# Performance work log

Measured on AMD Instinct MI355X. Metric: run time of the kernel, lower is better.

Reference implementation:

```python
import jax, jax.numpy as jnp
import numpy as np

PI = jnp.pi

def phasor_encode(x):
    # map phase in [-1,1] to unit complex phasor exp(i*pi*x)
    return jnp.exp(jnp.complex64(1j) * PI * x.astype(jnp.float32))

def phasor_act(z):
    # angle of complex activation, normalized back to [-1,1]
    return jnp.angle(z) / PI

def multi_dense(x, w, b):
    # PhasorMultiDense: x [b,t,d], w [h,d,D], b [h,D] (complex bias, ones init)
    xz = phasor_encode(x)                                      # [b,t,d] complex64
    wz = w.astype(jnp.complex64)
    bz = b.astype(jnp.complex64)
    yz = jnp.einsum('btd,hdD->bhtD', xz, wz) + bz[None, :, None, :]
    return phasor_act(yz)                                      # [b,h,t,D] real

def attend(q, k, v):
    # VSA phasor attention: similarity = Re(qz . conj(kz)) / d, softmax, complex bundle of v phasors
    d = q.shape[-1]
    qz = phasor_encode(q)
    kz = phasor_encode(k)
    scores = jnp.real(jnp.einsum('bhtd,bhTd->bhtT', qz, jnp.conj(kz))) / d
    probs = jax.nn.softmax(scores, axis=-1)
    vz = phasor_encode(v)
    out = jnp.einsum('bhtT,bhTd->bhtd', probs.astype(jnp.complex64), vz)
    return phasor_act(out)                                     # [b,h,t,D]

def setup_inputs() -> dict:
    key = jax.random.key(0)
    ks = jax.random.split(key, 8)
    B, Tq, Tkv, D, H = 2, 1024, 1024, 512, 8
    sw = 1.0 / np.sqrt(D)       # VarianceScaling(1.0) fan_in
    swo = 1.0 / np.sqrt(H * D)
    return {
        'query': jax.random.uniform(ks[0], (B, Tq, D), jnp.float32, -1.0, 1.0),
        'keyvalue': jax.random.uniform(ks[1], (B, Tkv, D), jnp.float32, -1.0, 1.0),
        'wq': jax.random.normal(ks[2], (H, D, D), jnp.float32) * sw,
        'bq': jnp.ones((H, D), jnp.float32),
        'wk': jax.random.normal(ks[3], (H, D, D), jnp.float32) * sw,
        'bk': jnp.ones((H, D), jnp.float32),
        'wv': jax.random.normal(ks[4], (H, D, D), jnp.float32) * sw,
        'bv': jnp.ones((H, D), jnp.float32),
        'wo': jax.random.normal(ks[5], (H * D, D), jnp.float32) * swo,
        'bo': jnp.ones((D,), jnp.float32),
    }

def reference(query, keyvalue, wq, bq, wk, bk, wv, bv, wo, bo):
    q = multi_dense(query, wq, bq)        # [b,h,t,D]
    k = multi_dense(keyvalue, wk, bk)
    v = multi_dense(keyvalue, wv, bv)
    r = attend(q, k, v)                   # [b,h,t,D]
    b_, h_, t_, d_ = r.shape
    r_flat = jnp.transpose(r, (0, 2, 1, 3)).reshape(b_, t_, h_ * d_)  # b t (h d)
    # final PhasorDense
    xz = phasor_encode(r_flat)
    z = jnp.einsum('btd,dD->btD', xz, wo.astype(jnp.complex64)) + bo.astype(jnp.complex64)
    return phasor_act(z)                  # [b, t_q, output_channels]
```

## Files before the change

### kernel.cpp

```cpp
#include <hip/hip_runtime.h>
#include <math.h>


#define PI_F 3.14159274101257324f

typedef __attribute__((ext_vector_type(8))) _Float16 half8;
typedef __attribute__((ext_vector_type(4))) _Float16 half4;
typedef __attribute__((ext_vector_type(2))) _Float16 half2v;
typedef __attribute__((ext_vector_type(16))) float f32x16;
typedef unsigned int u32;

#define MFMA32(a, b, c) __builtin_amdgcn_mfma_f32_32x32x16_f16((a), (b), (c), 0, 0, 0)
#define ROWOF(r, ln) (((r) & 3) + 8 * ((r) >> 2) + 4 * ((ln) >> 5))

__device__ __forceinline__ void gll16(const void* g, void* l) {
    __builtin_amdgcn_global_load_lds(
        (const __attribute__((address_space(1))) u32*)g,
        (__attribute__((address_space(3))) u32*)l, 16, 0, 0);
}

#define MKSRC(U, NT, gh, gl, stride, sp, dp, dbase)                         \
    _Pragma("unroll") for (int u_ = 0; u_ < (U); ++u_) {                    \
        const int idx_ = u_ * (NT) + tid;                                   \
        const int row_ = idx_ >> 3, ss_ = idx_ & 7;                         \
        const int sl_ = ss_ ^ (row_ & 7);                                   \
        sp[u_] = ((sl_ < 4) ? (gh) : (gl)) + (size_t)row_ * (stride)        \
                 + (sl_ & 3) * 8;                                           \
        dp[u_] = (dbase) + idx_ * 16;                                       \
    }
#define STAGE(U, sp, dp, bufoff, kk)                                        \
    _Pragma("unroll") for (int u_ = 0; u_ < (U); ++u_)                      \
        gll16(sp[u_] + (kk), lds + (bufoff) + dp[u_]);

__device__ __forceinline__ half8 fragP(const char* ldsp, int row, int oct, int hilo) {
    const int sl = (oct + hilo * 4) ^ (row & 7);
    return *(const half8*)(ldsp + row * 128 + (sl << 4));
}

__device__ __forceinline__ void split2(float x, _Float16& h, _Float16& l) {
    _Float16 hh = (_Float16)x;
    h = hh;
    l = (_Float16)((x - (float)hh) * 4096.0f);
}

__device__ __forceinline__ int xcdswz(int bid, int nwg) {
    const int cpx = nwg >> 3;
    return (bid & 7) * cpx + (bid >> 3);
}

__global__ __launch_bounds__(256) void encode_phasor(
    const float* __restrict__ x,
    _Float16* __restrict__ ch, _Float16* __restrict__ cl,
    _Float16* __restrict__ sh, _Float16* __restrict__ sl)
{
    const int idx = blockIdx.x * 256 + threadIdx.x;
    float4 v = ((const float4*)x)[idx];
    float cc[4], ss[4];
    sincosf(PI_F * v.x, &ss[0], &cc[0]);
    sincosf(PI_F * v.y, &ss[1], &cc[1]);
    sincosf(PI_F * v.z, &ss[2], &cc[2]);
    sincosf(PI_F * v.w, &ss[3], &cc[3]);
    half4 chv, clv, shv, slv;
#pragma unroll
    for (int q = 0; q < 4; ++q) {
        _Float16 a, b;
        split2(cc[q], a, b); chv[q] = a; clv[q] = b;
        split2(ss[q], a, b); shv[q] = a; slv[q] = b;
    }
    ((half4*)ch)[idx] = chv;
    ((half4*)cl)[idx] = clv;
    ((half4*)sh)[idx] = shv;
    ((half4*)sl)[idx] = slv;
}

__global__ __launch_bounds__(256) void tsplit64(
    const float* __restrict__ w, _Float16* __restrict__ th, _Float16* __restrict__ tl,
    int K, int N)
{
    const int kt = blockIdx.x, ntile = blockIdx.y, h = blockIdx.z;
    const int k0 = kt * 64, n0 = ntile * 64;
    __shared__ float T[64][65];
    const int tid = threadIdx.x;
    const float* wb = w + (size_t)h * K * N;
    {
        const int r = tid >> 4, c4 = (tid & 15) * 4;
#pragma unroll
        for (int rr = 0; rr < 64; rr += 16) {
            float4 v = *(const float4*)&wb[(size_t)(k0 + rr + r) * N + n0 + c4];
            T[rr + r][c4 + 0] = v.x; T[rr + r][c4 + 1] = v.y;
            T[rr + r][c4 + 2] = v.z; T[rr + r][c4 + 3] = v.w;
        }
    }
    __syncthreads();
    {
        const int n = tid >> 2, kq = (tid & 3) * 16;
        half8 hv[2], lv[2];
#pragma unroll
        for (int q = 0; q < 16; ++q) {
            float f = T[kq + q][n];
            _Float16 hh, ll; split2(f, hh, ll);
            hv[q >> 3][q & 7] = hh; lv[q >> 3][q & 7] = ll;
        }
        _Float16* oh = th + ((size_t)h * N + n0 + n) * K + k0 + kq;
        _Float16* ol = tl + ((size_t)h * N + n0 + n) * K + k0 + kq;
        *(half8*)oh = hv[0]; *(half8*)(oh + 8) = hv[1];
        *(half8*)ol = lv[0]; *(half8*)(ol + 8) = lv[1];
    }
}

__global__ __launch_bounds__(256, 2) void proj_qk(
    const _Float16* __restrict__ qch, const _Float16* __restrict__ qcl,
    const _Float16* __restrict__ qsh, const _Float16* __restrict__ qsl,
    const _Float16* __restrict__ kch, const _Float16* __restrict__ kcl,
    const _Float16* __restrict__ ksh, const _Float16* __restrict__ ksl,
    const _Float16* __restrict__ wqh, const _Float16* __restrict__ wql,
    const _Float16* __restrict__ wkh, const _Float16* __restrict__ wkl,
    const float* __restrict__ bq, const float* __restrict__ bk,
    _Float16* __restrict__ qzh, _Float16* __restrict__ qzl,
    _Float16* __restrict__ kzh, _Float16* __restrict__ kzl,
    int h0, int hcnt)
{
    const int inp = blockIdx.z;
    const _Float16* xch = inp ? kch : qch;
    const _Float16* xcl = inp ? kcl : qcl;
    const _Float16* xsh = inp ? ksh : qsh;
    const _Float16* xsl = inp ? ksl : qsl;
    const _Float16* wth = inp ? wkh : wqh;
    const _Float16* wtl = inp ? wkl : wql;
    const float* bias = inp ? bk : bq;
    _Float16* ozh = inp ? kzh : qzh;
    _Float16* ozl = inp ? kzl : qzl;

    const int m0 = blockIdx.x * 64;
    const int hc = blockIdx.y >> 2;
    const int n0 = (blockIdx.y & 3) * 128;
    __shared__ char lds[65536];
    const int tid = threadIdx.x, wv = tid >> 6, ln = tid & 63;
    const int wr = wv >> 1, wc = wv & 1, lm32 = ln & 31, lh = ln >> 5;

    const _Float16* sp_xc[2]; int dp_xc[2];
    const _Float16* sp_xs[2]; int dp_xs[2];
    const _Float16* sp_w[4];  int dp_w[4];
    MKSRC(2, 256, xch + (size_t)m0 * 512, xcl + (size_t)m0 * 512, 512, sp_xc, dp_xc, 0);
    MKSRC(2, 256, xsh + (size_t)m0 * 512, xsl + (size_t)m0 * 512, 512, sp_xs, dp_xs, 8192);
    const _Float16* wbh = wth + ((size_t)hc * 512 + n0) * 512;
    const _Float16* wbl = wtl + ((size_t)hc * 512 + n0) * 512;
    MKSRC(4, 256, wbh, wbl, 512, sp_w, dp_w, 16384);

    f32x16 ach[2] = {}, acl[2] = {}, ash[2] = {}, asl[2] = {};

    STAGE(2, sp_xc, dp_xc, 0, 0);
    STAGE(2, sp_xs, dp_xs, 0, 0);
    STAGE(4, sp_w,  dp_w,  0, 0);
    int off = 0;
    for (int s = 0; s < 16; ++s) {
        __syncthreads();
        const int nxt = off ^ 32768;
        if (s + 1 < 16) {
            const int kk = (s + 1) * 32;
            STAGE(2, sp_xc, dp_xc, nxt, kk);
            STAGE(2, sp_xs, dp_xs, nxt, kk);
            STAGE(4, sp_w,  dp_w,  nxt, kk);
        }
        const char* Xc = lds + off;
        const char* Xs = lds + off + 8192;
        const char* W  = lds + off + 16384;
        __builtin_amdgcn_s_setprio(1);
#pragma unroll
        for (int kw = 0; kw < 2; ++kw) {
            const int oct = kw * 2 + lh;
            half8 wh0 = fragP(W, wc * 64 + lm32, oct, 0);
            half8 wh1 = fragP(W, wc * 64 + 32 + lm32, oct, 0);
            half8 wl0 = fragP(W, wc * 64 + lm32, oct, 1);
            half8 wl1 = fragP(W, wc * 64 + 32 + lm32, oct, 1);
            half8 c1 = fragP(Xc, wr * 32 + lm32, oct, 0);
            half8 c2 = fragP(Xc, wr * 32 + lm32, oct, 1);
            half8 s1 = fragP(Xs, wr * 32 + lm32, oct, 0);
            half8 s2 = fragP(Xs, wr * 32 + lm32, oct, 1);
            ach[0] = MFMA32(c1, wh0, ach[0]);
            acl[0] = MFMA32(c1, wl0, acl[0]);
            acl[0] = MFMA32(c2, wh0, acl[0]);
            ash[0] = MFMA32(s1, wh0, ash[0]);
            asl[0] = MFMA32(s1, wl0, asl[0]);
            asl[0] = MFMA32(s2, wh0, asl[0]);
            ach[1] = MFMA32(c1, wh1, ach[1]);
            acl[1] = MFMA32(c1, wl1, acl[1]);
            acl[1] = MFMA32(c2, wh1, acl[1]);
            ash[1] = MFMA32(s1, wh1, ash[1]);
            asl[1] = MFMA32(s1, wl1, asl[1]);
            asl[1] = MFMA32(s2, wh1, asl[1]);
        }
        __builtin_amdgcn_s_setprio(0);
        off = nxt;
    }

    const float LS = 1.0f / 4096.0f;
    const int b = m0 >> 10, tbase = m0 & 1023;
    const size_t zz = (size_t)(b * hcnt + hc);
#pragma unroll
    for (int j = 0; j < 2; ++j) {
        const int nloc = wc * 64 + j * 32 + lm32;
        const float bval = bias[(size_t)(h0 + hc) * 512 + n0 + nloc];
#pragma unroll
        for (int r = 0; r < 16; ++r) {
            const int mloc = wr * 32 + ROWOF(r, ln);
            float yc = ach[j][r] + acl[j][r] * LS + bval;
            float ys = ash[j][r] + asl[j][r] * LS;
            float inv = 1.0f / sqrtf(fmaxf(yc * yc + ys * ys, 1e-36f));
            float c = yc * inv, sn = ys * inv;
            _Float16 chh, chl, shh, shl;
            split2(c, chh, chl); split2(sn, shh, shl);
            const size_t offo = (zz * 1024 + tbase + mloc) * 1024 + 2 * (n0 + nloc);
            half2v hv, lv;
            hv[0] = chh; hv[1] = shh; lv[0] = chl; lv[1] = shl;
            *(half2v*)(ozh + offo) = hv;
            *(half2v*)(ozl + offo) = lv;
        }
    }
}

__global__ __launch_bounds__(256, 2) void proj_v(
    const _Float16* __restrict__ xch, const _Float16* __restrict__ xcl,
    const _Float16* __restrict__ xsh, const _Float16* __restrict__ xsl,
    const _Float16* __restrict__ wth, const _Float16* __restrict__ wtl,
    const float* __restrict__ bias,
    _Float16* __restrict__ vch, _Float16* __restrict__ vcl,
    _Float16* __restrict__ vsh, _Float16* __restrict__ vsl,
    int h0, int hcnt)
{
    const int m0 = blockIdx.x * 64;
    const int hc = blockIdx.y >> 2;
    const int n0 = (blockIdx.y & 3) * 128;
    __shared__ char lds[65536];
    const int tid = threadIdx.x, wv = tid >> 6, ln = tid & 63;
    const int wr = wv >> 1, wc = wv & 1, lm32 = ln & 31, lh = ln >> 5;

    const _Float16* sp_xc[2]; int dp_xc[2];
    const _Float16* sp_xs[2]; int dp_xs[2];
    const _Float16* sp_w[4];  int dp_w[4];
    MKSRC(2, 256, xch + (size_t)m0 * 512, xcl + (size_t)m0 * 512, 512, sp_xc, dp_xc, 0);
    MKSRC(2, 256, xsh + (size_t)m0 * 512, xsl + (size_t)m0 * 512, 512, sp_xs, dp_xs, 8192);
    const _Float16* wbh = wth + ((size_t)hc * 512 + n0) * 512;
    const _Float16* wbl = wtl + ((size_t)hc * 512 + n0) * 512;
    MKSRC(4, 256, wbh, wbl, 512, sp_w, dp_w, 16384);

    f32x16 ach[2] = {}, acl[2] = {}, ash[2] = {}, asl[2] = {};

    STAGE(2, sp_xc, dp_xc, 0, 0);
    STAGE(2, sp_xs, dp_xs, 0, 0);
    STAGE(4, sp_w,  dp_w,  0, 0);
    int off = 0;
    for (int s = 0; s < 16; ++s) {
        __syncthreads();
        const int nxt = off ^ 32768;
        if (s + 1 < 16) {
            const int kk = (s + 1) * 32;
            STAGE(2, sp_xc, dp_xc, nxt, kk);
            STAGE(2, sp_xs, dp_xs, nxt, kk);
            STAGE(4, sp_w,  dp_w,  nxt, kk);
        }
        const char* Xc = lds + off;
        const char* Xs = lds + off + 8192;
        const char* W  = lds + off + 16384;
        __builtin_amdgcn_s_setprio(1);
#pragma unroll
        for (int kw = 0; kw < 2; ++kw) {
            const int oct = kw * 2 + lh;
            half8 wh0 = fragP(W, wc * 64 + lm32, oct, 0);
            half8 wh1 = fragP(W, wc * 64 + 32 + lm32, oct, 0);
            half8 wl0 = fragP(W, wc * 64 + lm32, oct, 1);
            half8 wl1 = fragP(W, wc * 64 + 32 + lm32, oct, 1);
            half8 c1 = fragP(Xc, wr * 32 + lm32, oct, 0);
            half8 c2 = fragP(Xc, wr * 32 + lm32, oct, 1);
            half8 s1 = fragP(Xs, wr * 32 + lm32, oct, 0);
            half8 s2 = fragP(Xs, wr * 32 + lm32, oct, 1);
            ach[0] = MFMA32(c1, wh0, ach[0]);
            acl[0] = MFMA32(c1, wl0, acl[0]);
            acl[0] = MFMA32(c2, wh0, acl[0]);
            ash[0] = MFMA32(s1, wh0, ash[0]);
            asl[0] = MFMA32(s1, wl0, asl[0]);
            asl[0] = MFMA32(s2, wh0, asl[0]);
            ach[1] = MFMA32(c1, wh1, ach[1]);
            acl[1] = MFMA32(c1, wl1, acl[1]);
            acl[1] = MFMA32(c2, wh1, acl[1]);
            ash[1] = MFMA32(s1, wh1, ash[1]);
            asl[1] = MFMA32(s1, wl1, asl[1]);
            asl[1] = MFMA32(s2, wh1, asl[1]);
        }
        __builtin_amdgcn_s_setprio(0);
        off = nxt;
    }

    const float LS = 1.0f / 4096.0f;
    const int b = m0 >> 10, tbase = m0 & 1023;
    const size_t zz = (size_t)(b * hcnt + hc);
    _Float16* T = (_Float16*)lds;
#pragma unroll
    for (int round = 0; round < 2; ++round) {
        __syncthreads();
#pragma unroll
        for (int j = 0; j < 2; ++j) {
            const int dloc = wc * 64 + j * 32 + lm32;
            const float bval = bias[(size_t)(h0 + hc) * 512 + n0 + dloc];
#pragma unroll
            for (int r = 0; r < 16; ++r) {
                const int tloc = wr * 32 + ROWOF(r, ln);
                float yc = ach[j][r] + acl[j][r] * LS + bval;
                float ys = ash[j][r] + asl[j][r] * LS;
                float inv = 1.0f / sqrtf(fmaxf(yc * yc + ys * ys, 1e-36f));
                float val = (round ? ys : yc) * inv;
                _Float16 hh, ll;
                split2(val, hh, ll);
                T[dloc * 72 + tloc] = hh;
                T[9216 + dloc * 72 + tloc] = ll;
            }
        }
        __syncthreads();
        {
            const int p2 = tid >> 7, d = tid & 127;
            const _Float16* src = T + p2 * 9216 + d * 72;
            _Float16* plane = (round == 0) ? (p2 ? vcl : vch) : (p2 ? vsl : vsh);
            _Float16* dst = plane + (zz * 512 + n0 + d) * 1024 + tbase;
#pragma unroll
            for (int q = 0; q < 8; ++q)
                *(half8*)(dst + q * 8) = *(const half8*)(src + q * 8);
        }
    }
}

__global__ __launch_bounds__(256, 2) void scores_mfma(
    const _Float16* __restrict__ qzh, const _Float16* __restrict__ qzl,
    const _Float16* __restrict__ kzh, const _Float16* __restrict__ kzl,
    float* __restrict__ S, int Z)
{
    const int wg = xcdswz(blockIdx.x, Z * 64);
    const int z = wg >> 6;
    const int rem = wg & 63;
    const int m0 = (rem & 7) << 7, n0 = (rem >> 3) << 7;
    __shared__ char lds[65536];
    const size_t zb = (size_t)z << 20;
    const int tid = threadIdx.x, wv = tid >> 6, ln = tid & 63;
    const int wr = wv >> 1, wc = wv & 1, lm32 = ln & 31, lh = ln >> 5;

    const _Float16* sp_a[4]; int dp_a[4];
    const _Float16* sp_b[4]; int dp_b[4];
    MKSRC(4, 256, qzh + zb + (size_t)m0 * 1024, qzl + zb + (size_t)m0 * 1024, 1024, sp_a, dp_a, 0);
    MKSRC(4, 256, kzh + zb + (size_t)n0 * 1024, kzl + zb + (size_t)n0 * 1024, 1024, sp_b, dp_b, 16384);

    f32x16 acch[2][2] = {}, accl[2][2] = {};

    STAGE(4, sp_a, dp_a, 0, 0);
    STAGE(4, sp_b, dp_b, 0, 0);
    int off = 0;
    for (int s = 0; s < 32; ++s) {
        __syncthreads();
        const int nxt = off ^ 32768;
        if (s + 1 < 32) {
            const int kk = (s + 1) * 32;
            STAGE(4, sp_a, dp_a, nxt, kk);
            STAGE(4, sp_b, dp_b, nxt, kk);
        }
        const char* A  = lds + off;
        const char* Bb = lds + off + 16384;
        __builtin_amdgcn_s_setprio(1);
#pragma unroll
        for (int kw = 0; kw < 2; ++kw) {
            const int oct = kw * 2 + lh;
            half8 bh0 = fragP(Bb, wc * 64 + lm32, oct, 0);
            half8 bh1 = fragP(Bb, wc * 64 + 32 + lm32, oct, 0);
            half8 bl0 = fragP(Bb, wc * 64 + lm32, oct, 1);
            half8 bl1 = fragP(Bb, wc * 64 + 32 + lm32, oct, 1);
#pragma unroll
            for (int i = 0; i < 2; ++i) {
                half8 qh = fragP(A, wr * 64 + i * 32 + lm32, oct, 0);
                half8 ql = fragP(A, wr * 64 + i * 32 + lm32, oct, 1);
                acch[i][0] = MFMA32(qh, bh0, acch[i][0]);
                accl[i][0] = MFMA32(qh, bl0, accl[i][0]);
                accl[i][0] = MFMA32(ql, bh0, accl[i][0]);
                acch[i][1] = MFMA32(qh, bh1, acch[i][1]);
                accl[i][1] = MFMA32(qh, bl1, accl[i][1]);
                accl[i][1] = MFMA32(ql, bh1, accl[i][1]);
            }
        }
        __builtin_amdgcn_s_setprio(0);
        off = nxt;
    }
    const float LS = 1.0f / 4096.0f, SC = 1.0f / 512.0f;
#pragma unroll
    for (int i = 0; i < 2; ++i)
#pragma unroll
        for (int j = 0; j < 2; ++j)
#pragma unroll
            for (int r = 0; r < 16; ++r) {
                const int row = m0 + wr * 64 + i * 32 + ROWOF(r, ln);
                const int col = n0 + wc * 64 + j * 32 + lm32;
                S[zb + (size_t)row * 1024 + col] =
                    (acch[i][j][r] + accl[i][j][r] * LS) * SC;
            }
}

__global__ __launch_bounds__(256) void softmax_split(float* __restrict__ S)
{
    const size_t row = blockIdx.x;
    float* p = S + row * 1024;
    const int tid = threadIdx.x;
    float4 v = ((const float4*)p)[tid];
    float m = fmaxf(fmaxf(v.x, v.y), fmaxf(v.z, v.w));
#pragma unroll
    for (int off = 32; off >= 1; off >>= 1)
        m = fmaxf(m, __shfl_xor(m, off));
    __shared__ float redm[4], reds[4];
    const int wid = tid >> 6, lane = tid & 63;
    if (lane == 0) redm[wid] = m;
    __syncthreads();
    m = fmaxf(fmaxf(redm[0], redm[1]), fmaxf(redm[2], redm[3]));
    float4 e;
    e.x = expf(v.x - m); e.y = expf(v.y - m);
    e.z = expf(v.z - m); e.w = expf(v.w - m);
    float s = (e.x + e.y) + (e.z + e.w);
#pragma unroll
    for (int off = 32; off >= 1; off >>= 1)
        s += __shfl_xor(s, off);
    if (lane == 0) reds[wid] = s;
    __syncthreads();
    s = (reds[0] + reds[1]) + (reds[2] + reds[3]);
    e.x /= s; e.y /= s; e.z /= s; e.w /= s;
    __syncthreads();
    _Float16* ph = (_Float16*)p;
    half4 hv, lv;
    _Float16 a, b;
    split2(e.x, a, b); hv[0] = a; lv[0] = b;
    split2(e.y, a, b); hv[1] = a; lv[1] = b;
    split2(e.z, a, b); hv[2] = a; lv[2] = b;
    split2(e.w, a, b); hv[3] = a; lv[3] = b;
    *(half4*)(ph + tid * 4) = hv;
    *(half4*)(ph + 1024 + tid * 4) = lv;
}

__global__ __launch_bounds__(256, 2) void pv_mfma(
    const _Float16* __restrict__ P,
    const _Float16* __restrict__ vch, const _Float16* __restrict__ vcl,
    const _Float16* __restrict__ vsh, const _Float16* __restrict__ vsl,
    _Float16* __restrict__ rch, _Float16* __restrict__ rcl,
    _Float16* __restrict__ rsh, _Float16* __restrict__ rsl,
    int h0, int hcnt, int Z)
{
    const int wg = xcdswz(blockIdx.x, Z * 64);
    const int z = wg >> 6;
    const int rem = wg & 63;
    const int m0 = (rem & 7) << 7, n0 = (rem >> 3) << 6;
    __shared__ char lds[65536];
    const int tid = threadIdx.x, wv = tid >> 6, ln = tid & 63;
    const int wr = wv >> 1, wc = wv & 1, lm32 = ln & 31, lh = ln >> 5;

    const _Float16* Pb = P + (size_t)z * 1024 * 2048 + (size_t)m0 * 2048;
    const size_t vb = (size_t)z * 512 * 1024 + (size_t)n0 * 1024;
    const _Float16* sp_p[4];  int dp_p[4];
    const _Float16* sp_vc[2]; int dp_vc[2];
    const _Float16* sp_vs[2]; int dp_vs[2];
    MKSRC(4, 256, Pb, Pb + 1024, 2048, sp_p, dp_p, 0);
    MKSRC(2, 256, vch + vb, vcl + vb, 1024, sp_vc, dp_vc, 16384);
    MKSRC(2, 256, vsh + vb, vsl + vb, 1024, sp_vs, dp_vs, 24576);

    f32x16 ac_h[2] = {}, ac_l[2] = {}, as_h[2] = {}, as_l[2] = {};

    STAGE(4, sp_p,  dp_p,  0, 0);
    STAGE(2, sp_vc, dp_vc, 0, 0);
    STAGE(2, sp_vs, dp_vs, 0, 0);
    int off = 0;
    for (int s = 0; s < 32; ++s) {
        __syncthreads();
        const int nxt = off ^ 32768;
        if (s + 1 < 32) {
            const int kk = (s + 1) * 32;
            STAGE(4, sp_p,  dp_p,  nxt, kk);
            STAGE(2, sp_vc, dp_vc, nxt, kk);
            STAGE(2, sp_vs, dp_vs, nxt, kk);
        }
        const char* A  = lds + off;
        const char* Vc = lds + off + 16384;
        const char* Vs = lds + off + 24576;
        __builtin_amdgcn_s_setprio(1);
#pragma unroll
        for (int kw = 0; kw < 2; ++kw) {
            const int oct = kw * 2 + lh;
            half8 vc1 = fragP(Vc, wc * 32 + lm32, oct, 0);
            half8 vc2 = fragP(Vc, wc * 32 + lm32, oct, 1);
            half8 vs1 = fragP(Vs, wc * 32 + lm32, oct, 0);
            half8 vs2 = fragP(Vs, wc * 32 + lm32, oct, 1);
#pragma unroll
            for (int i = 0; i < 2; ++i) {
                half8 ph = fragP(A, wr * 64 + i * 32 + lm32, oct, 0);
                half8 pl = fragP(A, wr * 64 + i * 32 + lm32, oct, 1);
                ac_h[i] = MFMA32(ph, vc1, ac_h[i]);
                ac_l[i] = MFMA32(ph, vc2, ac_l[i]);
                ac_l[i] = MFMA32(pl, vc1, ac_l[i]);
                as_h[i] = MFMA32(ph, vs1, as_h[i]);
                as_l[i] = MFMA32(ph, vs2, as_l[i]);
                as_l[i] = MFMA32(pl, vs1, as_l[i]);
            }
        }
        __builtin_amdgcn_s_setprio(0);
        off = nxt;
    }
    const float LS = 1.0f / 4096.0f;
    const int b = z / hcnt, hg = h0 + z % hcnt;
#pragma unroll
    for (int i = 0; i < 2; ++i)
#pragma unroll
        for (int r = 0; r < 16; ++r) {
            const int t = m0 + wr * 64 + i * 32 + ROWOF(r, ln);
            const int d = n0 + wc * 32 + lm32;
            float zc = ac_h[i][r] + ac_l[i][r] * LS;
            float zs = as_h[i][r] + as_l[i][r] * LS;
            float inv = 1.0f / sqrtf(fmaxf(zc * zc + zs * zs, 1e-36f));
            float c = zc * inv, sn = zs * inv;
            _Float16 chh, chl, shh, shl;
            split2(c, chh, chl); split2(sn, shh, shl);
            const size_t offo = ((size_t)(b * 1024 + t)) * 4096 + (size_t)hg * 512 + d;
            rch[offo] = chh; rcl[offo] = chl; rsh[offo] = shh; rsl[offo] = shl;
        }
}

__global__ __launch_bounds__(256, 2) void final_mfma(
    const _Float16* __restrict__ rch, const _Float16* __restrict__ rcl,
    const _Float16* __restrict__ rsh, const _Float16* __restrict__ rsl,
    const _Float16* __restrict__ woh, const _Float16* __restrict__ wol,
    float* __restrict__ pbuf)
{
    const int m0 = blockIdx.x * 64, n0 = blockIdx.y * 128;
    const int ks = blockIdx.z;
    const size_t kbase = (size_t)ks * 1024;
    __shared__ char lds[65536];
    const int tid = threadIdx.x, wv = tid >> 6, ln = tid & 63;
    const int wr = wv >> 1, wc = wv & 1, lm32 = ln & 31, lh = ln >> 5;

    const _Float16* sp_rc[2]; int dp_rc[2];
    const _Float16* sp_rs[2]; int dp_rs[2];
    const _Float16* sp_w[4];  int dp_w[4];
    MKSRC(2, 256, rch + (size_t)m0 * 4096 + kbase, rcl + (size_t)m0 * 4096 + kbase, 4096, sp_rc, dp_rc, 0);
    MKSRC(2, 256, rsh + (size_t)m0 * 4096 + kbase, rsl + (size_t)m0 * 4096 + kbase, 4096, sp_rs, dp_rs, 8192);
    MKSRC(4, 256, woh + (size_t)n0 * 4096 + kbase, wol + (size_t)n0 * 4096 + kbase, 4096, sp_w, dp_w, 16384);

    f32x16 rr_h[2] = {}, rr_l[2] = {}, ri_h[2] = {}, ri_l[2] = {};

    STAGE(2, sp_rc, dp_rc, 0, 0);
    STAGE(2, sp_rs, dp_rs, 0, 0);
    STAGE(4, sp_w,  dp_w,  0, 0);
    int off = 0;
    for (int s = 0; s < 32; ++s) {
        __syncthreads();
        const int nxt = off ^ 32768;
        if (s + 1 < 32) {
            const int kk = (s + 1) * 32;
            STAGE(2, sp_rc, dp_rc, nxt, kk);
            STAGE(2, sp_rs, dp_rs, nxt, kk);
            STAGE(4, sp_w,  dp_w,  nxt, kk);
        }
        const char* Rc = lds + off;
        const char* Rs = lds + off + 8192;
        const char* W  = lds + off + 16384;
        __builtin_amdgcn_s_setprio(1);
#pragma unroll
        for (int kw = 0; kw < 2; ++kw) {
            const int oct = kw * 2 + lh;
            half8 wh0 = fragP(W, wc * 64 + lm32, oct, 0);
            half8 wh1 = fragP(W, wc * 64 + 32 + lm32, oct, 0);
            half8 wl0 = fragP(W, wc * 64 + lm32, oct, 1);
            half8 wl1 = fragP(W, wc * 64 + 32 + lm32, oct, 1);
            half8 c1 = fragP(Rc, wr * 32 + lm32, oct, 0);
            half8 c2 = fragP(Rc, wr * 32 + lm32, oct, 1);
            half8 s1 = fragP(Rs, wr * 32 + lm32, oct, 0);
            half8 s2 = fragP(Rs, wr * 32 + lm32, oct, 1);
            rr_h[0] = MFMA32(c1, wh0, rr_h[0]);
            rr_l[0] = MFMA32(c1, wl0, rr_l[0]);
            rr_l[0] = MFMA32(c2, wh0, rr_l[0]);
            ri_h[0] = MFMA32(s1, wh0, ri_h[0]);
            ri_l[0] = MFMA32(s1, wl0, ri_l[0]);
            ri_l[0] = MFMA32(s2, wh0, ri_l[0]);
            rr_h[1] = MFMA32(c1, wh1, rr_h[1]);
            rr_l[1] = MFMA32(c1, wl1, rr_l[1]);
            rr_l[1] = MFMA32(c2, wh1, rr_l[1]);
            ri_h[1] = MFMA32(s1, wh1, ri_h[1]);
            ri_l[1] = MFMA32(s1, wl1, ri_l[1]);
            ri_l[1] = MFMA32(s2, wh1, ri_l[1]);
        }
        __builtin_amdgcn_s_setprio(0);
        off = nxt;
    }
    const float LS = 1.0f / 4096.0f;
#pragma unroll
    for (int j = 0; j < 2; ++j) {
        const int ng = n0 + wc * 64 + j * 32 + lm32;
#pragma unroll
        for (int r = 0; r < 16; ++r) {
            const int mg = m0 + wr * 32 + ROWOF(r, ln);
            float zr = rr_h[j][r] + rr_l[j][r] * LS;
            float zi = ri_h[j][r] + ri_l[j][r] * LS;
            float2 v; v.x = zr; v.y = zi;
            *(float2*)&pbuf[((size_t)(ks * 2048 + mg) * 512 + ng) * 2] = v;
        }
    }
}

__global__ __launch_bounds__(256) void final_combine(
    const float* __restrict__ pbuf, const float* __restrict__ bo,
    float* __restrict__ out, int KS)
{
    const int m = blockIdx.x, t = threadIdx.x;
    float4 acc = {0.f, 0.f, 0.f, 0.f};
    for (int s = 0; s < KS; ++s) {
        float4 v = *(const float4*)&pbuf[(size_t)(s * 2048 + m) * 1024 + t * 4];
        acc.x += v.x; acc.y += v.y; acc.z += v.z; acc.w += v.w;
    }
    const int n0 = t * 2;
    out[(size_t)m * 512 + n0]     = atan2f(acc.y, acc.x + bo[n0]) / PI_F;
    out[(size_t)m * 512 + n0 + 1] = atan2f(acc.w, acc.z + bo[n0 + 1]) / PI_F;
}

extern "C" void kernel_launch(void* const* d_in, const int* in_sizes, int n_in,
                              void* d_out, int out_size, void* d_ws, size_t ws_size,
                              hipStream_t stream)
{
    (void)in_sizes; (void)n_in; (void)out_size;
    const float* query    = (const float*)d_in[0];
    const float* keyvalue = (const float*)d_in[1];
    const float* wq = (const float*)d_in[2];
    const float* bq = (const float*)d_in[3];
    const float* wk = (const float*)d_in[4];
    const float* bk = (const float*)d_in[5];
    const float* wv = (const float*)d_in[6];
    const float* bv = (const float*)d_in[7];
    const float* wo = (const float*)d_in[8];
    const float* bo = (const float*)d_in[9];
    float* out = (float*)d_out;

    int hcnt;
    if (ws_size >= (size_t)320 * 1024 * 1024) hcnt = 8;
    else if (ws_size >= (size_t)240 * 1024 * 1024) hcnt = 4;
    else hcnt = 2;
    const int Z = 2 * hcnt;
    const int KS = (hcnt == 2) ? 2 : 4;

    char* p = (char*)d_ws;
    auto alloc = [&](size_t bytes) {
        char* r = p;
        p += (bytes + 255) & ~(size_t)255;
        return r;
    };
    const size_t PLX = (size_t)2048 * 512;
    _Float16* xq[4]; for (int i = 0; i < 4; ++i) xq[i] = (_Float16*)alloc(PLX * 2);
    _Float16* xk[4]; for (int i = 0; i < 4; ++i) xk[i] = (_Float16*)alloc(PLX * 2);
    _Float16* woT[2]; for (int i = 0; i < 2; ++i) woT[i] = (_Float16*)alloc((size_t)512 * 4096 * 2);
    const size_t WTE = (size_t)hcnt * 512 * 512;
    _Float16* wqT[2]; for (int i = 0; i < 2; ++i) wqT[i] = (_Float16*)alloc(WTE * 2);
    _Float16* wkT[2]; for (int i = 0; i < 2; ++i) wkT[i] = (_Float16*)alloc(WTE * 2);
    _Float16* wvT[2]; for (int i = 0; i < 2; ++i) wvT[i] = (_Float16*)alloc(WTE * 2);
    const size_t QZE = (size_t)Z * 1024 * 1024;
    _Float16* qz[2]; for (int i = 0; i < 2; ++i) qz[i] = (_Float16*)alloc(QZE * 2);
    _Float16* kz[2]; for (int i = 0; i < 2; ++i) kz[i] = (_Float16*)alloc(QZE * 2);
    float* S = (float*)alloc(QZE * 4);
    const size_t VTE = (size_t)Z * 512 * 1024;
    _Float16* vT[4]; for (int i = 0; i < 4; ++i) vT[i] = (_Float16*)alloc(VTE * 2);
    const size_t RCE = (size_t)2048 * 4096;
    _Float16* rcs[4];
    if (hcnt == 8) {
        for (int i = 0; i < 4; ++i) rcs[i] = (_Float16*)((char*)qz[0] + (size_t)i * RCE * 2);
    } else {
        for (int i = 0; i < 4; ++i) rcs[i] = (_Float16*)alloc(RCE * 2);
    }
    float* pbuf = (float*)kz[0];

    dim3 blk(256);

    encode_phasor<<<1024, blk, 0, stream>>>(query, xq[0], xq[1], xq[2], xq[3]);
    encode_phasor<<<1024, blk, 0, stream>>>(keyvalue, xk[0], xk[1], xk[2], xk[3]);
    tsplit64<<<dim3(64, 8, 1), blk, 0, stream>>>(wo, woT[0], woT[1], 4096, 512);

    for (int c = 0; c < 8 / hcnt; ++c) {
        const int h0 = c * hcnt;
        const float* wqc = wq + (size_t)h0 * 512 * 512;
        const float* wkc = wk + (size_t)h0 * 512 * 512;
        const float* wvc = wv + (size_t)h0 * 512 * 512;
        tsplit64<<<dim3(8, 8, hcnt), blk, 0, stream>>>(wqc, wqT[0], wqT[1], 512, 512);
        tsplit64<<<dim3(8, 8, hcnt), blk, 0, stream>>>(wkc, wkT[0], wkT[1], 512, 512);
        tsplit64<<<dim3(8, 8, hcnt), blk, 0, stream>>>(wvc, wvT[0], wvT[1], 512, 512);

        proj_qk<<<dim3(32, 4 * hcnt, 2), blk, 0, stream>>>(
            xq[0], xq[1], xq[2], xq[3], xk[0], xk[1], xk[2], xk[3],
            wqT[0], wqT[1], wkT[0], wkT[1], bq, bk,
            qz[0], qz[1], kz[0], kz[1], h0, hcnt);
        proj_v<<<dim3(32, 4 * hcnt), blk, 0, stream>>>(
            xk[0], xk[1], xk[2], xk[3], wvT[0], wvT[1], bv,
            vT[0], vT[1], vT[2], vT[3], h0, hcnt);

        scores_mfma<<<dim3(Z * 64), blk, 0, stream>>>(qz[0], qz[1], kz[0], kz[1], S, Z);
        softmax_split<<<dim3(Z * 1024), blk, 0, stream>>>(S);
        pv_mfma<<<dim3(Z * 64), blk, 0, stream>>>(
            (const _Float16*)S, vT[0], vT[1], vT[2], vT[3],
            rcs[0], rcs[1], rcs[2], rcs[3], h0, hcnt, Z);
    }

    final_mfma<<<dim3(32, 4, KS), blk, 0, stream>>>(
        rcs[0], rcs[1], rcs[2], rcs[3], woT[0], woT[1], pbuf);
    final_combine<<<dim3(2048), blk, 0, stream>>>(pbuf, bo, out, KS);
}
```

Measured before the change: 579.9 us.

## Use 512-thread blocks with triple-buffered LDS pipeline in all MFMA GEMM kernels

All the MFMA GEMM kernels (projections, scores, PV, final) now use 512-thread blocks with wider N tiles. Staging moves from a double-buffered swizzled layout to a three-slot ring of pre-fragmented LDS tiles, prefetched three k-steps ahead with explicit vmcnt waits and split barriers. Each k-step's fragments go into registers before the next prefetch is issued. This aims to hide global-load latency and halve redundant reloads of the X tiles, at the cost of 144KB of LDS per block, which likely caps occupancy at one block per CU despite the launch bound of 2. It also raises register pressure.

```diff
diff --git a/kernel.cpp b/kernel.cpp
--- a/kernel.cpp
+++ b/kernel.cpp
@@ -19,24 +19,6 @@
         (__attribute__((address_space(3))) u32*)l, 16, 0, 0);
 }
 
-#define MKSRC(U, NT, gh, gl, stride, sp, dp, dbase)                         \
-    _Pragma("unroll") for (int u_ = 0; u_ < (U); ++u_) {                    \
-        const int idx_ = u_ * (NT) + tid;                                   \
-        const int row_ = idx_ >> 3, ss_ = idx_ & 7;                         \
-        const int sl_ = ss_ ^ (row_ & 7);                                   \
-        sp[u_] = ((sl_ < 4) ? (gh) : (gl)) + (size_t)row_ * (stride)        \
-                 + (sl_ & 3) * 8;                                           \
-        dp[u_] = (dbase) + idx_ * 16;                                       \
-    }
-#define STAGE(U, sp, dp, bufoff, kk)                                        \
-    _Pragma("unroll") for (int u_ = 0; u_ < (U); ++u_)                      \
-        gll16(sp[u_] + (kk), lds + (bufoff) + dp[u_]);
-
-__device__ __forceinline__ half8 fragP(const char* ldsp, int row, int oct, int hilo) {
-    const int sl = (oct + hilo * 4) ^ (row & 7);
-    return *(const half8*)(ldsp + row * 128 + (sl << 4));
-}
-
 __device__ __forceinline__ void split2(float x, _Float16& h, _Float16& l) {
     _Float16 hh = (_Float16)x;
     h = hh;
@@ -47,6 +29,26 @@
     const int cpx = nwg >> 3;
     return (bid & 7) * cpx + (bid >> 3);
 }
+
+#define SLOT 49152
+
+#define ISSUE6(slotoff, kk)                                                  \
+    _Pragma("unroll") for (int u_ = 0; u_ < 6; ++u_)                         \
+        gll16(sp[u_] + (kk), lds + (slotoff) + dp[u_]);
+
+#define PIPE_WAIT(s, NS)                                                     \
+    if ((s) + 3 <= (NS))      asm volatile("s_waitcnt vmcnt(12)" ::: "memory"); \
+    else if ((s) + 2 == (NS)) asm volatile("s_waitcnt vmcnt(6)" ::: "memory");  \
+    else                      asm volatile("s_waitcnt vmcnt(0)" ::: "memory");  \
+    __builtin_amdgcn_s_barrier();                                            \
+    __builtin_amdgcn_sched_barrier(0);
+
+#define PIPE_MID(s, NS)                                                      \
+    asm volatile("s_waitcnt lgkmcnt(0)" ::: "memory");                       \
+    __builtin_amdgcn_sched_barrier(0);                                       \
+    __builtin_amdgcn_s_barrier();                                            \
+    __builtin_amdgcn_sched_barrier(0);                                       \
+    if ((s) + 3 < (NS)) { ISSUE6(off, ((s) + 3) * 64); }
 
 __global__ __launch_bounds__(256) void encode_phasor(
     const float* __restrict__ x,
@@ -108,7 +110,7 @@
     }
 }
 
-__global__ __launch_bounds__(256, 2) void proj_qk(
+__global__ __launch_bounds__(512, 2) void proj_qk(
     const _Float16* __restrict__ qch, const _Float16* __restrict__ qcl,
     const _Float16* __restrict__ qsh, const _Float16* __restrict__ qsl,
     const _Float16* __restrict__ kch, const _Float16* __restrict__ kcl,
@@ -132,66 +134,64 @@
     _Float16* ozl = inp ? kzl : qzl;
 
     const int m0 = blockIdx.x * 64;
-    const int hc = blockIdx.y >> 2;
-    const int n0 = (blockIdx.y & 3) * 128;
-    __shared__ char lds[65536];
+    const int hc = blockIdx.y >> 1;
+    const int n0h = (blockIdx.y & 1) * 256;
+    __shared__ char lds[147456];
     const int tid = threadIdx.x, wv = tid >> 6, ln = tid & 63;
-    const int wr = wv >> 1, wc = wv & 1, lm32 = ln & 31, lh = ln >> 5;
-
-    const _Float16* sp_xc[2]; int dp_xc[2];
-    const _Float16* sp_xs[2]; int dp_xs[2];
-    const _Float16* sp_w[4];  int dp_w[4];
-    MKSRC(2, 256, xch + (size_t)m0 * 512, xcl + (size_t)m0 * 512, 512, sp_xc, dp_xc, 0);
-    MKSRC(2, 256, xsh + (size_t)m0 * 512, xsl + (size_t)m0 * 512, 512, sp_xs, dp_xs, 8192);
-    const _Float16* wbh = wth + ((size_t)hc * 512 + n0) * 512;
-    const _Float16* wbl = wtl + ((size_t)hc * 512 + n0) * 512;
-    MKSRC(4, 256, wbh, wbl, 512, sp_w, dp_w, 16384);
+    const int wr = wv >> 2, wc = wv & 3, lm32 = ln & 31;
+
+    const char* sp[6]; int dp[6];
+#pragma unroll
+    for (int u = 0; u < 6; ++u) {
+        const int g = u * 8 + wv;
+        const _Float16 *ph, *pl; int row0, stride; int f;
+        if (g < 8)       { f = g;      ph = xch; pl = xcl; row0 = m0; stride = 512; }
+        else if (g < 16) { f = g - 8;  ph = xsh; pl = xsl; row0 = m0; stride = 512; }
+        else             { f = g - 16;
+                           ph = wth + (size_t)hc * 262144;
+                           pl = wtl + (size_t)hc * 262144;
+                           row0 = n0h; stride = 512; }
+        const int R = f >> 2, ks = (f >> 1) & 1, hl = f & 1;
+        sp[u] = (const char*)((hl ? pl : ph)
+                + (size_t)(row0 + R * 32 + (ln & 31)) * stride
+                + ks * 16 + (ln >> 5) * 8);
+        dp[u] = u * 8192 + tid * 16;
+    }
 
     f32x16 ach[2] = {}, acl[2] = {}, ash[2] = {}, asl[2] = {};
 
-    STAGE(2, sp_xc, dp_xc, 0, 0);
-    STAGE(2, sp_xs, dp_xs, 0, 0);
-    STAGE(4, sp_w,  dp_w,  0, 0);
+    ISSUE6(0, 0); ISSUE6(SLOT, 64); ISSUE6(2 * SLOT, 128);
     int off = 0;
-    for (int s = 0; s < 16; ++s) {
-        __syncthreads();
-        const int nxt = off ^ 32768;
-        if (s + 1 < 16) {
-            const int kk = (s + 1) * 32;
-            STAGE(2, sp_xc, dp_xc, nxt, kk);
-            STAGE(2, sp_xs, dp_xs, nxt, kk);
-            STAGE(4, sp_w,  dp_w,  nxt, kk);
-        }
-        const char* Xc = lds + off;
-        const char* Xs = lds + off + 8192;
-        const char* W  = lds + off + 16384;
+    const int NS = 16;
+    for (int s = 0; s < NS; ++s) {
+        PIPE_WAIT(s, NS);
+        half8 xc[2][2], xs[2][2], w[2][2][2];
+#pragma unroll
+        for (int ks = 0; ks < 2; ++ks)
+#pragma unroll
+            for (int hl = 0; hl < 2; ++hl) {
+                xc[ks][hl] = *(const half8*)(lds + off + (wr * 4 + ks * 2 + hl) * 1024 + ln * 16);
+                xs[ks][hl] = *(const half8*)(lds + off + 8192 + (wr * 4 + ks * 2 + hl) * 1024 + ln * 16);
+#pragma unroll
+                for (int j = 0; j < 2; ++j)
+                    w[ks][j][hl] = *(const half8*)(lds + off + 16384
+                        + ((wc * 2 + j) * 4 + ks * 2 + hl) * 1024 + ln * 16);
+            }
+        PIPE_MID(s, NS);
         __builtin_amdgcn_s_setprio(1);
 #pragma unroll
-        for (int kw = 0; kw < 2; ++kw) {
-            const int oct = kw * 2 + lh;
-            half8 wh0 = fragP(W, wc * 64 + lm32, oct, 0);
-            half8 wh1 = fragP(W, wc * 64 + 32 + lm32, oct, 0);
-            half8 wl0 = fragP(W, wc * 64 + lm32, oct, 1);
-            half8 wl1 = fragP(W, wc * 64 + 32 + lm32, oct, 1);
-            half8 c1 = fragP(Xc, wr * 32 + lm32, oct, 0);
-            half8 c2 = fragP(Xc, wr * 32 + lm32, oct, 1);
-            half8 s1 = fragP(Xs, wr * 32 + lm32, oct, 0);
-            half8 s2 = fragP(Xs, wr * 32 + lm32, oct, 1);
-            ach[0] = MFMA32(c1, wh0, ach[0]);
-            acl[0] = MFMA32(c1, wl0, acl[0]);
-            acl[0] = MFMA32(c2, wh0, acl[0]);
-            ash[0] = MFMA32(s1, wh0, ash[0]);
-            asl[0] = MFMA32(s1, wl0, asl[0]);
-            asl[0] = MFMA32(s2, wh0, asl[0]);
-            ach[1] = MFMA32(c1, wh1, ach[1]);
-            acl[1] = MFMA32(c1, wl1, acl[1]);
-            acl[1] = MFMA32(c2, wh1, acl[1]);
-            ash[1] = MFMA32(s1, wh1, ash[1]);
-            asl[1] = MFMA32(s1, wl1, asl[1]);
-            asl[1] = MFMA32(s2, wh1, asl[1]);
-        }
+        for (int ks = 0; ks < 2; ++ks)
+#pragma unroll
+            for (int j = 0; j < 2; ++j) {
+                ach[j] = MFMA32(xc[ks][0], w[ks][j][0], ach[j]);
+                acl[j] = MFMA32(xc[ks][0], w[ks][j][1], acl[j]);
+                acl[j] = MFMA32(xc[ks][1], w[ks][j][0], acl[j]);
+                ash[j] = MFMA32(xs[ks][0], w[ks][j][0], ash[j]);
+                asl[j] = MFMA32(xs[ks][0], w[ks][j][1], asl[j]);
+                asl[j] = MFMA32(xs[ks][1], w[ks][j][0], asl[j]);
+            }
         __builtin_amdgcn_s_setprio(0);
-        off = nxt;
+        off = (off == 2 * SLOT) ? 0 : off + SLOT;
     }
 
     const float LS = 1.0f / 4096.0f;
@@ -200,7 +200,7 @@
 #pragma unroll
     for (int j = 0; j < 2; ++j) {
         const int nloc = wc * 64 + j * 32 + lm32;
-        const float bval = bias[(size_t)(h0 + hc) * 512 + n0 + nloc];
+        const float bval = bias[(size_t)(h0 + hc) * 512 + n0h + nloc];
 #pragma unroll
         for (int r = 0; r < 16; ++r) {
             const int mloc = wr * 32 + ROWOF(r, ln);
@@ -210,7 +210,7 @@
             float c = yc * inv, sn = ys * inv;
             _Float16 chh, chl, shh, shl;
             split2(c, chh, chl); split2(sn, shh, shl);
-            const size_t offo = (zz * 1024 + tbase + mloc) * 1024 + 2 * (n0 + nloc);
+            const size_t offo = (zz * 1024 + tbase + mloc) * 1024 + 2 * (n0h + nloc);
             half2v hv, lv;
             hv[0] = chh; hv[1] = shh; lv[0] = chl; lv[1] = shl;
             *(half2v*)(ozh + offo) = hv;
@@ -219,7 +219,7 @@
     }
 }
 
-__global__ __launch_bounds__(256, 2) void proj_v(
+__global__ __launch_bounds__(512, 2) void proj_v(
     const _Float16* __restrict__ xch, const _Float16* __restrict__ xcl,
     const _Float16* __restrict__ xsh, const _Float16* __restrict__ xsl,
     const _Float16* __restrict__ wth, const _Float16* __restrict__ wtl,
@@ -229,161 +229,166 @@
     int h0, int hcnt)
 {
     const int m0 = blockIdx.x * 64;
-    const int hc = blockIdx.y >> 2;
-    const int n0 = (blockIdx.y & 3) * 128;
-    __shared__ char lds[65536];
+    const int hc = blockIdx.y >> 1;
+    const int n0h = (blockIdx.y & 1) * 256;
+    __shared__ char lds[147456];
     const int tid = threadIdx.x, wv = tid >> 6, ln = tid & 63;
-    const int wr = wv >> 1, wc = wv & 1, lm32 = ln & 31, lh = ln >> 5;
-
-    const _Float16* sp_xc[2]; int dp_xc[2];
-    const _Float16* sp_xs[2]; int dp_xs[2];
-    const _Float16* sp_w[4];  int dp_w[4];
-    MKSRC(2, 256, xch + (size_t)m0 * 512, xcl + (size_t)m0 * 512, 512, sp_xc, dp_xc, 0);
-    MKSRC(2, 256, xsh + (size_t)m0 * 512, xsl + (size_t)m0 * 512, 512, sp_xs, dp_xs, 8192);
-    const _Float16* wbh = wth + ((size_t)hc * 512 + n0) * 512;
-    const _Float16* wbl = wtl + ((size_t)hc * 512 + n0) * 512;
-    MKSRC(4, 256, wbh, wbl, 512, sp_w, dp_w, 16384);
+    const int wr = wv >> 2, wc = wv & 3, lm32 = ln & 31;
+
+    const char* sp[6]; int dp[6];
+#pragma unroll
+    for (int u = 0; u < 6; ++u) {
+        const int g = u * 8 + wv;
+        const _Float16 *ph, *pl; int row0, stride; int f;
+        if (g < 8)       { f = g;      ph = xch; pl = xcl; row0 = m0; stride = 512; }
+        else if (g < 16) { f = g - 8;  ph = xsh; pl = xsl; row0 = m0; stride = 512; }
+        else             { f = g - 16;
+                           ph = wth + (size_t)hc * 262144;
+                           pl = wtl + (size_t)hc * 262144;
+                           row0 = n0h; stride = 512; }
+        const int R = f >> 2, ks = (f >> 1) & 1, hl = f & 1;
+        sp[u] = (const char*)((hl ? pl : ph)
+                + (size_t)(row0 + R * 32 + (ln & 31)) * stride
+                + ks * 16 + (ln >> 5) * 8);
+        dp[u] = u * 8192 + tid * 16;
+    }
 
     f32x16 ach[2] = {}, acl[2] = {}, ash[2] = {}, asl[2] = {};
 
-    STAGE(2, sp_xc, dp_xc, 0, 0);
-    STAGE(2, sp_xs, dp_xs, 0, 0);
-    STAGE(4, sp_w,  dp_w,  0, 0);
+    ISSUE6(0, 0); ISSUE6(SLOT, 64); ISSUE6(2 * SLOT, 128);
     int off = 0;
-    for (int s = 0; s < 16; ++s) {
-        __syncthreads();
-        const int nxt = off ^ 32768;
-        if (s + 1 < 16) {
-            const int kk = (s + 1) * 32;
-            STAGE(2, sp_xc, dp_xc, nxt, kk);
-            STAGE(2, sp_xs, dp_xs, nxt, kk);
-            STAGE(4, sp_w,  dp_w,  nxt, kk);
-        }
-        const char* Xc = lds + off;
-        const char* Xs = lds + off + 8192;
-        const char* W  = lds + off + 16384;
+    const int NS = 16;
+    for (int s = 0; s < NS; ++s) {
+        PIPE_WAIT(s, NS);
+        half8 xc[2][2], xs[2][2], w[2][2][2];
+#pragma unroll
+        for (int ks = 0; ks < 2; ++ks)
+#pragma unroll
+            for (int hl = 0; hl < 2; ++hl) {
+                xc[ks][hl] = *(const half8*)(lds + off + (wr * 4 + ks * 2 + hl) * 1024 + ln * 16);
+                xs[ks][hl] = *(const half8*)(lds + off + 8192 + (wr * 4 + ks * 2 + hl) * 1024 + ln * 16);
+#pragma unroll
+                for (int j = 0; j < 2; ++j)
+                    w[ks][j][hl] = *(const half8*)(lds + off + 16384
+                        + ((wc * 2 + j) * 4 + ks * 2 + hl) * 1024 + ln * 16);
+            }
+        PIPE_MID(s, NS);
         __builtin_amdgcn_s_setprio(1);
 #pragma unroll
-        for (int kw = 0; kw < 2; ++kw) {
-            const int oct = kw * 2 + lh;
-            half8 wh0 = fragP(W, wc * 64 + lm32, oct, 0);
-            half8 wh1 = fragP(W, wc * 64 + 32 + lm32, oct, 0);
-            half8 wl0 = fragP(W, wc * 64 + lm32, oct, 1);
-            half8 wl1 = fragP(W, wc * 64 + 32 + lm32, oct, 1);
-            half8 c1 = fragP(Xc, wr * 32 + lm32, oct, 0);
-            half8 c2 = fragP(Xc, wr * 32 + lm32, oct, 1);
-            half8 s1 = fragP(Xs, wr * 32 + lm32, oct, 0);
-            half8 s2 = fragP(Xs, wr * 32 + lm32, oct, 1);
-            ach[0] = MFMA32(c1, wh0, ach[0]);
-            acl[0] = MFMA32(c1, wl0, acl[0]);
-            acl[0] = MFMA32(c2, wh0, acl[0]);
-            ash[0] = MFMA32(s1, wh0, ash[0]);
-            asl[0] = MFMA32(s1, wl0, asl[0]);
-            asl[0] = MFMA32(s2, wh0, asl[0]);
-            ach[1] = MFMA32(c1, wh1, ach[1]);
-            acl[1] = MFMA32(c1, wl1, acl[1]);
-            acl[1] = MFMA32(c2, wh1, acl[1]);
-            ash[1] = MFMA32(s1, wh1, ash[1]);
-            asl[1] = MFMA32(s1, wl1, asl[1]);
-            asl[1] = MFMA32(s2, wh1, asl[1]);
-        }
+        for (int ks = 0; ks < 2; ++ks)
+#pragma unroll
+            for (int j = 0; j < 2; ++j) {
+                ach[j] = MFMA32(xc[ks][0], w[ks][j][0], ach[j]);
+                acl[j] = MFMA32(xc[ks][0], w[ks][j][1], acl[j]);
+                acl[j] = MFMA32(xc[ks][1], w[ks][j][0], acl[j]);
+                ash[j] = MFMA32(xs[ks][0], w[ks][j][0], ash[j]);
+                asl[j] = MFMA32(xs[ks][0], w[ks][j][1], asl[j]);
+                asl[j] = MFMA32(xs[ks][1], w[ks][j][0], asl[j]);
+            }
         __builtin_amdgcn_s_setprio(0);
-        off = nxt;
+        off = (off == 2 * SLOT) ? 0 : off + SLOT;
     }
 
     const float LS = 1.0f / 4096.0f;
     const int b = m0 >> 10, tbase = m0 & 1023;
     const size_t zz = (size_t)(b * hcnt + hc);
-    _Float16* T = (_Float16*)lds;
-#pragma unroll
-    for (int round = 0; round < 2; ++round) {
-        __syncthreads();
-#pragma unroll
-        for (int j = 0; j < 2; ++j) {
-            const int dloc = wc * 64 + j * 32 + lm32;
-            const float bval = bias[(size_t)(h0 + hc) * 512 + n0 + dloc];
-#pragma unroll
-            for (int r = 0; r < 16; ++r) {
-                const int tloc = wr * 32 + ROWOF(r, ln);
-                float yc = ach[j][r] + acl[j][r] * LS + bval;
-                float ys = ash[j][r] + asl[j][r] * LS;
-                float inv = 1.0f / sqrtf(fmaxf(yc * yc + ys * ys, 1e-36f));
-                float val = (round ? ys : yc) * inv;
-                _Float16 hh, ll;
-                split2(val, hh, ll);
-                T[dloc * 72 + tloc] = hh;
-                T[9216 + dloc * 72 + tloc] = ll;
-            }
+    __syncthreads();
+#pragma unroll
+    for (int j = 0; j < 2; ++j) {
+        const int dloc = wc * 64 + j * 32 + lm32;
+        const float bval = bias[(size_t)(h0 + hc) * 512 + n0h + dloc];
+#pragma unroll
+        for (int r = 0; r < 16; ++r) {
+            const int tloc = wr * 32 + ROWOF(r, ln);
+            float yc = ach[j][r] + acl[j][r] * LS + bval;
+            float ys = ash[j][r] + asl[j][r] * LS;
+            float inv = 1.0f / sqrtf(fmaxf(yc * yc + ys * ys, 1e-36f));
+            float c = yc * inv, sn = ys * inv;
+            _Float16 chh, chl, shh, shl;
+            split2(c, chh, chl); split2(sn, shh, shl);
+            ((_Float16*)(lds +      0))[dloc * 72 + tloc] = chh;
+            ((_Float16*)(lds +  36864))[dloc * 72 + tloc] = chl;
+            ((_Float16*)(lds +  73728))[dloc * 72 + tloc] = shh;
+            ((_Float16*)(lds + 110592))[dloc * 72 + tloc] = shl;
         }
-        __syncthreads();
-        {
-            const int p2 = tid >> 7, d = tid & 127;
-            const _Float16* src = T + p2 * 9216 + d * 72;
-            _Float16* plane = (round == 0) ? (p2 ? vcl : vch) : (p2 ? vsl : vsh);
-            _Float16* dst = plane + (zz * 512 + n0 + d) * 1024 + tbase;
+    }
+    __syncthreads();
+    {
+        const int p = tid >> 7;
+        _Float16* outp = (p == 0) ? vch : (p == 1) ? vcl : (p == 2) ? vsh : vsl;
+        const int dl = (tid & 127) * 2;
+#pragma unroll
+        for (int dd = 0; dd < 2; ++dd) {
+            const _Float16* srcT = (const _Float16*)(lds + p * 36864) + (dl + dd) * 72;
+            _Float16* dst = outp + (zz * 512 + n0h + dl + dd) * 1024 + tbase;
 #pragma unroll
             for (int q = 0; q < 8; ++q)
-                *(half8*)(dst + q * 8) = *(const half8*)(src + q * 8);
+                *(half8*)(dst + q * 8) = *(const half8*)(srcT + q * 8);
         }
     }
 }
 
-__global__ __launch_bounds__(256, 2) void scores_mfma(
+__global__ __launch_bounds__(512, 2) void scores_mfma(
     const _Float16* __restrict__ qzh, const _Float16* __restrict__ qzl,
     const _Float16* __restrict__ kzh, const _Float16* __restrict__ kzl,
     float* __restrict__ S, int Z)
 {
-    const int wg = xcdswz(blockIdx.x, Z * 64);
-    const int z = wg >> 6;
-    const int rem = wg & 63;
-    const int m0 = (rem & 7) << 7, n0 = (rem >> 3) << 7;
-    __shared__ char lds[65536];
+    const int wg = xcdswz(blockIdx.x, Z * 32);
+    const int z = wg >> 5;
+    const int rem = wg & 31;
+    const int m0 = (rem & 7) << 7, n0 = (rem >> 3) << 8;
+    __shared__ char lds[147456];
     const size_t zb = (size_t)z << 20;
     const int tid = threadIdx.x, wv = tid >> 6, ln = tid & 63;
-    const int wr = wv >> 1, wc = wv & 1, lm32 = ln & 31, lh = ln >> 5;
-
-    const _Float16* sp_a[4]; int dp_a[4];
-    const _Float16* sp_b[4]; int dp_b[4];
-    MKSRC(4, 256, qzh + zb + (size_t)m0 * 1024, qzl + zb + (size_t)m0 * 1024, 1024, sp_a, dp_a, 0);
-    MKSRC(4, 256, kzh + zb + (size_t)n0 * 1024, kzl + zb + (size_t)n0 * 1024, 1024, sp_b, dp_b, 16384);
+    const int wr = wv >> 2, wc = wv & 3, lm32 = ln & 31;
+
+    const char* sp[6]; int dp[6];
+#pragma unroll
+    for (int u = 0; u < 6; ++u) {
+        const int g = u * 8 + wv;
+        const _Float16 *ph, *pl; int row0; int f;
+        if (g < 16) { f = g;      ph = qzh + zb; pl = qzl + zb; row0 = m0; }
+        else        { f = g - 16; ph = kzh + zb; pl = kzl + zb; row0 = n0; }
+        const int R = f >> 2, ks = (f >> 1) & 1, hl = f & 1;
+        sp[u] = (const char*)((hl ? pl : ph)
+                + (size_t)(row0 + R * 32 + (ln & 31)) * 1024
+                + ks * 16 + (ln >> 5) * 8);
+        dp[u] = u * 8192 + tid * 16;
+    }
 
     f32x16 acch[2][2] = {}, accl[2][2] = {};
 
-    STAGE(4, sp_a, dp_a, 0, 0);
-    STAGE(4, sp_b, dp_b, 0, 0);
+    ISSUE6(0, 0); ISSUE6(SLOT, 64); ISSUE6(2 * SLOT, 128);
     int off = 0;
-    for (int s = 0; s < 32; ++s) {
-        __syncthreads();
-        const int nxt = off ^ 32768;
-        if (s + 1 < 32) {
-            const int kk = (s + 1) * 32;
-            STAGE(4, sp_a, dp_a, nxt, kk);
-            STAGE(4, sp_b, dp_b, nxt, kk);
-        }
-        const char* A  = lds + off;
-        const char* Bb = lds + off + 16384;
+    const int NS = 32;
+    for (int s = 0; s < NS; ++s) {
+        PIPE_WAIT(s, NS);
+        half8 ah[2][2], al[2][2], bh[2][2], bl[2][2];
+#pragma unroll
+        for (int ks = 0; ks < 2; ++ks)
+#pragma unroll
+            for (int i = 0; i < 2; ++i) {
+                const int Ra = (wr * 2 + i) * 4 + ks * 2;
+                ah[ks][i] = *(const half8*)(lds + off + Ra * 1024 + ln * 16);
+                al[ks][i] = *(const half8*)(lds + off + (Ra + 1) * 1024 + ln * 16);
+                const int Rb = (wc * 2 + i) * 4 + ks * 2;
+                bh[ks][i] = *(const half8*)(lds + off + 16384 + Rb * 1024 + ln * 16);
+                bl[ks][i] = *(const half8*)(lds + off + 16384 + (Rb + 1) * 1024 + ln * 16);
+            }
+        PIPE_MID(s, NS);
         __builtin_amdgcn_s_setprio(1);
 #pragma unroll
-        for (int kw = 0; kw < 2; ++kw) {
-            const int oct = kw * 2 + lh;
-            half8 bh0 = fragP(Bb, wc * 64 + lm32, oct, 0);
-            half8 bh1 = fragP(Bb, wc * 64 + 32 + lm32, oct, 0);
-            half8 bl0 = fragP(Bb, wc * 64 + lm32, oct, 1);
-            half8 bl1 = fragP(Bb, wc * 64 + 32 + lm32, oct, 1);
-#pragma unroll
-            for (int i = 0; i < 2; ++i) {
-                half8 qh = fragP(A, wr * 64 + i * 32 + lm32, oct, 0);
-                half8 ql = fragP(A, wr * 64 + i * 32 + lm32, oct, 1);
-                acch[i][0] = MFMA32(qh, bh0, acch[i][0]);
-                accl[i][0] = MFMA32(qh, bl0, accl[i][0]);
-                accl[i][0] = MFMA32(ql, bh0, accl[i][0]);
-                acch[i][1] = MFMA32(qh, bh1, acch[i][1]);
-                accl[i][1] = MFMA32(qh, bl1, accl[i][1]);
-                accl[i][1] = MFMA32(ql, bh1, accl[i][1]);
-            }
-        }
+        for (int ks = 0; ks < 2; ++ks)
+#pragma unroll
+            for (int i = 0; i < 2; ++i)
+#pragma unroll
+                for (int j = 0; j < 2; ++j) {
+                    acch[i][j] = MFMA32(ah[ks][i], bh[ks][j], acch[i][j]);
+                    accl[i][j] = MFMA32(ah[ks][i], bl[ks][j], accl[i][j]);
+                    accl[i][j] = MFMA32(al[ks][i], bh[ks][j], accl[i][j]);
+                }
         __builtin_amdgcn_s_setprio(0);
-        off = nxt;
+        off = (off == 2 * SLOT) ? 0 : off + SLOT;
     }
     const float LS = 1.0f / 4096.0f, SC = 1.0f / 512.0f;
 #pragma unroll
@@ -437,7 +442,7 @@
     *(half4*)(ph + 1024 + tid * 4) = lv;
 }
 
-__global__ __launch_bounds__(256, 2) void pv_mfma(
+__global__ __launch_bounds__(512, 2) void pv_mfma(
     const _Float16* __restrict__ P,
     const _Float16* __restrict__ vch, const _Float16* __restrict__ vcl,
     const _Float16* __restrict__ vsh, const _Float16* __restrict__ vsl,
@@ -445,63 +450,68 @@
     _Float16* __restrict__ rsh, _Float16* __restrict__ rsl,
     int h0, int hcnt, int Z)
 {
-    const int wg = xcdswz(blockIdx.x, Z * 64);
-    const int z = wg >> 6;
-    const int rem = wg & 63;
-    const int m0 = (rem & 7) << 7, n0 = (rem >> 3) << 6;
-    __shared__ char lds[65536];
+    const int wg = xcdswz(blockIdx.x, Z * 32);
+    const int z = wg >> 5;
+    const int rem = wg & 31;
+    const int m0 = (rem & 7) << 7, n0 = (rem >> 3) << 7;
+    __shared__ char lds[147456];
     const int tid = threadIdx.x, wv = tid >> 6, ln = tid & 63;
-    const int wr = wv >> 1, wc = wv & 1, lm32 = ln & 31, lh = ln >> 5;
-
-    const _Float16* Pb = P + (size_t)z * 1024 * 2048 + (size_t)m0 * 2048;
-    const size_t vb = (size_t)z * 512 * 1024 + (size_t)n0 * 1024;
-    const _Float16* sp_p[4];  int dp_p[4];
-    const _Float16* sp_vc[2]; int dp_vc[2];
-    const _Float16* sp_vs[2]; int dp_vs[2];
-    MKSRC(4, 256, Pb, Pb + 1024, 2048, sp_p, dp_p, 0);
-    MKSRC(2, 256, vch + vb, vcl + vb, 1024, sp_vc, dp_vc, 16384);
-    MKSRC(2, 256, vsh + vb, vsl + vb, 1024, sp_vs, dp_vs, 24576);
+    const int wr = wv >> 2, wc = wv & 3, lm32 = ln & 31;
+
+    const _Float16* Pb = P + (size_t)z * 1024 * 2048;
+    const size_t vb = (size_t)z * 512 * 1024;
+    const char* sp[6]; int dp[6];
+#pragma unroll
+    for (int u = 0; u < 6; ++u) {
+        const int g = u * 8 + wv;
+        const _Float16 *ph, *pl; int row0, stride; int f;
+        if (g < 16)      { f = g;      ph = Pb; pl = Pb + 1024; row0 = m0; stride = 2048; }
+        else if (g < 32) { f = g - 16; ph = vch + vb; pl = vcl + vb; row0 = n0; stride = 1024; }
+        else             { f = g - 32; ph = vsh + vb; pl = vsl + vb; row0 = n0; stride = 1024; }
+        const int R = f >> 2, ks = (f >> 1) & 1, hl = f & 1;
+        sp[u] = (const char*)((hl ? pl : ph)
+                + (size_t)(row0 + R * 32 + (ln & 31)) * stride
+                + ks * 16 + (ln >> 5) * 8);
+        dp[u] = u * 8192 + tid * 16;
+    }
 
     f32x16 ac_h[2] = {}, ac_l[2] = {}, as_h[2] = {}, as_l[2] = {};
 
-    STAGE(4, sp_p,  dp_p,  0, 0);
-    STAGE(2, sp_vc, dp_vc, 0, 0);
-    STAGE(2, sp_vs, dp_vs, 0, 0);
+    ISSUE6(0, 0); ISSUE6(SLOT, 64); ISSUE6(2 * SLOT, 128);
     int off = 0;
-    for (int s = 0; s < 32; ++s) {
-        __syncthreads();
-        const int nxt = off ^ 32768;
-        if (s + 1 < 32) {
-            const int kk = (s + 1) * 32;
-            STAGE(4, sp_p,  dp_p,  nxt, kk);
-            STAGE(2, sp_vc, dp_vc, nxt, kk);
-            STAGE(2, sp_vs, dp_vs, nxt, kk);
+    const int NS = 32;
+    for (int s = 0; s < NS; ++s) {
+        PIPE_WAIT(s, NS);
+        half8 ph_[2][2], pl_[2][2], vc[2][2], vs[2][2];
+#pragma unroll
+        for (int ks = 0; ks < 2; ++ks) {
+#pragma unroll
+            for (int i = 0; i < 2; ++i) {
+                const int Ra = (wr * 2 + i) * 4 + ks * 2;
+                ph_[ks][i] = *(const half8*)(lds + off + Ra * 1024 + ln * 16);
+                pl_[ks][i] = *(const half8*)(lds + off + (Ra + 1) * 1024 + ln * 16);
+            }
+            const int Rv = wc * 4 + ks * 2;
+            vc[ks][0] = *(const half8*)(lds + off + 16384 + Rv * 1024 + ln * 16);
+            vc[ks][1] = *(const half8*)(lds + off + 16384 + (Rv + 1) * 1024 + ln * 16);
+            vs[ks][0] = *(const half8*)(lds + off + 32768 + Rv * 1024 + ln * 16);
+            vs[ks][1] = *(const half8*)(lds + off + 32768 + (Rv + 1) * 1024 + ln * 16);
         }
-        const char* A  = lds + off;
-        const char* Vc = lds + off + 16384;
-        const char* Vs = lds + off + 24576;
+        PIPE_MID(s, NS);
         __builtin_amdgcn_s_setprio(1);
 #pragma unroll
-        for (int kw = 0; kw < 2; ++kw) {
-            const int oct = kw * 2 + lh;
-            half8 vc1 = fragP(Vc, wc * 32 + lm32, oct, 0);
-            half8 vc2 = fragP(Vc, wc * 32 + lm32, oct, 1);
-            half8 vs1 = fragP(Vs, wc * 32 + lm32, oct, 0);
-            half8 vs2 = fragP(Vs, wc * 32 + lm32, oct, 1);
+        for (int ks = 0; ks < 2; ++ks)
 #pragma unroll
             for (int i = 0; i < 2; ++i) {
-                half8 ph = fragP(A, wr * 64 + i * 32 + lm32, oct, 0);
-                half8 pl = fragP(A, wr * 64 + i * 32 + lm32, oct, 1);
-                ac_h[i] = MFMA32(ph, vc1, ac_h[i]);
-                ac_l[i] = MFMA32(ph, vc2, ac_l[i]);
-                ac_l[i] = MFMA32(pl, vc1, ac_l[i]);
-                as_h[i] = MFMA32(ph, vs1, as_h[i]);
-                as_l[i] = MFMA32(ph, vs2, as_l[i]);
-                as_l[i] = MFMA32(pl, vs1, as_l[i]);
-            }
-        }
+                ac_h[i] = MFMA32(ph_[ks][i], vc[ks][0], ac_h[i]);
+                ac_l[i] = MFMA32(ph_[ks][i], vc[ks][1], ac_l[i]);
+                ac_l[i] = MFMA32(pl_[ks][i], vc[ks][0], ac_l[i]);
+                as_h[i] = MFMA32(ph_[ks][i], vs[ks][0], as_h[i]);
+                as_l[i] = MFMA32(ph_[ks][i], vs[ks][1], as_l[i]);
+                as_l[i] = MFMA32(pl_[ks][i], vs[ks][0], as_l[i]);
+            }
         __builtin_amdgcn_s_setprio(0);
-        off = nxt;
+        off = (off == 2 * SLOT) ? 0 : off + SLOT;
     }
     const float LS = 1.0f / 4096.0f;
     const int b = z / hcnt, hg = h0 + z % hcnt;
@@ -522,71 +532,68 @@
         }
 }
 
-__global__ __launch_bounds__(256, 2) void final_mfma(
+__global__ __launch_bounds__(512, 2) void final_mfma(
     const _Float16* __restrict__ rch, const _Float16* __restrict__ rcl,
     const _Float16* __restrict__ rsh, const _Float16* __restrict__ rsl,
     const _Float16* __restrict__ woh, const _Float16* __restrict__ wol,
     float* __restrict__ pbuf)
 {
-    const int m0 = blockIdx.x * 64, n0 = blockIdx.y * 128;
-    const int ks = blockIdx.z;
-    const size_t kbase = (size_t)ks * 1024;
-    __shared__ char lds[65536];
+    const int m0 = blockIdx.x * 64, n0 = blockIdx.y * 256;
+    const int kspl = blockIdx.z;
+    const size_t kbase = (size_t)kspl * 1024;
+    __shared__ char lds[147456];
     const int tid = threadIdx.x, wv = tid >> 6, ln = tid & 63;
-    const int wr = wv >> 1, wc = wv & 1, lm32 = ln & 31, lh = ln >> 5;
-
-    const _Float16* sp_rc[2]; int dp_rc[2];
-    const _Float16* sp_rs[2]; int dp_rs[2];
-    const _Float16* sp_w[4];  int dp_w[4];
-    MKSRC(2, 256, rch + (size_t)m0 * 4096 + kbase, rcl + (size_t)m0 * 4096 + kbase, 4096, sp_rc, dp_rc, 0);
-    MKSRC(2, 256, rsh + (size_t)m0 * 4096 + kbase, rsl + (size_t)m0 * 4096 + kbase, 4096, sp_rs, dp_rs, 8192);
-    MKSRC(4, 256, woh + (size_t)n0 * 4096 + kbase, wol + (size_t)n0 * 4096 + kbase, 4096, sp_w, dp_w, 16384);
+    const int wr = wv >> 2, wc = wv & 3, lm32 = ln & 31;
+
+    const char* sp[6]; int dp[6];
+#pragma unroll
+    for (int u = 0; u < 6; ++u) {
+        const int g = u * 8 + wv;
+        const _Float16 *ph, *pl; int row0; int f;
+        if (g < 8)       { f = g;      ph = rch + kbase; pl = rcl + kbase; row0 = m0; }
+        else if (g < 16) { f = g - 8;  ph = rsh + kbase; pl = rsl + kbase; row0 = m0; }
+        else             { f = g - 16; ph = woh + kbase; pl = wol + kbase; row0 = n0; }
+        const int R = f >> 2, ks = (f >> 1) & 1, hl = f & 1;
+        sp[u] = (const char*)((hl ? pl : ph)
+                + (size_t)(row0 + R * 32 + (ln & 31)) * 4096
+                + ks * 16 + (ln >> 5) * 8);
+        dp[u] = u * 8192 + tid * 16;
+    }
 
     f32x16 rr_h[2] = {}, rr_l[2] = {}, ri_h[2] = {}, ri_l[2] = {};
 
-    STAGE(2, sp_rc, dp_rc, 0, 0);
-    STAGE(2, sp_rs, dp_rs, 0, 0);
-    STAGE(4, sp_w,  dp_w,  0, 0);
+    ISSUE6(0, 0); ISSUE6(SLOT, 64); ISSUE6(2 * SLOT, 128);
     int off = 0;
-    for (int s = 0; s < 32; ++s) {
-        __syncthreads();
-        const int nxt = off ^ 32768;
-        if (s + 1 < 32) {
-            const int kk = (s + 1) * 32;
-            STAGE(2, sp_rc, dp_rc, nxt, kk);
-            STAGE(2, sp_rs, dp_rs, nxt, kk);
-            STAGE(4, sp_w,  dp_w,  nxt, kk);
-        }
-        const char* Rc = lds + off;
-        const char* Rs = lds + off + 8192;
-        const char* W  = lds + off + 16384;
+    const int NS = 32;
+    for (int s = 0; s < NS; ++s) {
+        PIPE_WAIT(s, NS);
+        half8 rc[2][2], rs[2][2], w[2][2][2];
+#pragma unroll
+        for (int ks = 0; ks < 2; ++ks)
+#pragma unroll
+            for (int hl = 0; hl < 2; ++hl) {
+                rc[ks][hl] = *(const half8*)(lds + off + (wr * 4 + ks * 2 + hl) * 1024 + ln * 16);
+                rs[ks][hl] = *(const half8*)(lds + off + 8192 + (wr * 4 + ks * 2 + hl) * 1024 + ln * 16);
+#pragma unroll
+                for (int j = 0; j < 2; ++j)
+                    w[ks][j][hl] = *(const half8*)(lds + off + 16384
+                        + ((wc * 2 + j) * 4 + ks * 2 + hl) * 1024 + ln * 16);
+            }
+        PIPE_MID(s, NS);
         __builtin_amdgcn_s_setprio(1);
 #pragma unroll
-        for (int kw = 0; kw < 2; ++kw) {
-            const int oct = kw * 2 + lh;
-            half8 wh0 = fragP(W, wc * 64 + lm32, oct, 0);
-            half8 wh1 = fragP(W, wc * 64 + 32 + lm32, oct, 0);
-            half8 wl0 = fragP(W, wc * 64 + lm32, oct, 1);
-            half8 wl1 = fragP(W, wc * 64 + 32 + lm32, oct, 1);
-            half8 c1 = fragP(Rc, wr * 32 + lm32, oct, 0);
-            half8 c2 = fragP(Rc, wr * 32 + lm32, oct, 1);
-            half8 s1 = fragP(Rs, wr * 32 + lm32, oct, 0);
-            half8 s2 = fragP(Rs, wr * 32 + lm32, oct, 1);
-            rr_h[0] = MFMA32(c1, wh0, rr_h[0]);
-            rr_l[0] = MFMA32(c1, wl0, rr_l[0]);
-            rr_l[0] = MFMA32(c2, wh0, rr_l[0]);
-            ri_h[0] = MFMA32(s1, wh0, ri_h[0]);
-            ri_l[0] = MFMA32(s1, wl0, ri_l[0]);
-            ri_l[0] = MFMA32(s2, wh0, ri_l[0]);
-            rr_h[1] = MFMA32(c1, wh1, rr_h[1]);
-            rr_l[1] = MFMA32(c1, wl1, rr_l[1]);
-            rr_l[1] = MFMA32(c2, wh1, rr_l[1]);
-            ri_h[1] = MFMA32(s1, wh1, ri_h[1]);
-            ri_l[1] = MFMA32(s1, wl1, ri_l[1]);
-            ri_l[1] = MFMA32(s2, wh1, ri_l[1]);
-        }
+        for (int ks = 0; ks < 2; ++ks)
+#pragma unroll
+            for (int j = 0; j < 2; ++j) {
+                rr_h[j] = MFMA32(rc[ks][0], w[ks][j][0], rr_h[j]);
+                rr_l[j] = MFMA32(rc[ks][0], w[ks][j][1], rr_l[j]);
+                rr_l[j] = MFMA32(rc[ks][1], w[ks][j][0], rr_l[j]);
+                ri_h[j] = MFMA32(rs[ks][0], w[ks][j][0], ri_h[j]);
+                ri_l[j] = MFMA32(rs[ks][0], w[ks][j][1], ri_l[j]);
+                ri_l[j] = MFMA32(rs[ks][1], w[ks][j][0], ri_l[j]);
+            }
         __builtin_amdgcn_s_setprio(0);
-        off = nxt;
+        off = (off == 2 * SLOT) ? 0 : off + SLOT;
     }
     const float LS = 1.0f / 4096.0f;
 #pragma unroll
@@ -598,7 +605,7 @@
             float zr = rr_h[j][r] + rr_l[j][r] * LS;
             float zi = ri_h[j][r] + ri_l[j][r] * LS;
             float2 v; v.x = zr; v.y = zi;
-            *(float2*)&pbuf[((size_t)(ks * 2048 + mg) * 512 + ng) * 2] = v;
+            *(float2*)&pbuf[((size_t)(kspl * 2048 + mg) * 512 + ng) * 2] = v;
         }
     }
 }
@@ -671,7 +678,7 @@
     }
     float* pbuf = (float*)kz[0];
 
-    dim3 blk(256);
+    dim3 blk(256), blk5(512);
 
     encode_phasor<<<1024, blk, 0, stream>>>(query, xq[0], xq[1], xq[2], xq[3]);
     encode_phasor<<<1024, blk, 0, stream>>>(keyvalue, xk[0], xk[1], xk[2], xk[3]);
@@ -686,22 +693,22 @@
         tsplit64<<<dim3(8, 8, hcnt), blk, 0, stream>>>(wkc, wkT[0], wkT[1], 512, 512);
         tsplit64<<<dim3(8, 8, hcnt), blk, 0, stream>>>(wvc, wvT[0], wvT[1], 512, 512);
 
-        proj_qk<<<dim3(32, 4 * hcnt, 2), blk, 0, stream>>>(
+        proj_qk<<<dim3(32, hcnt * 2, 2), blk5, 0, stream>>>(
             xq[0], xq[1], xq[2], xq[3], xk[0], xk[1], xk[2], xk[3],
             wqT[0], wqT[1], wkT[0], wkT[1], bq, bk,
             qz[0], qz[1], kz[0], kz[1], h0, hcnt);
-        proj_v<<<dim3(32, 4 * hcnt), blk, 0, stream>>>(
+        proj_v<<<dim3(32, hcnt * 2), blk5, 0, stream>>>(
             xk[0], xk[1], xk[2], xk[3], wvT[0], wvT[1], bv,
             vT[0], vT[1], vT[2], vT[3], h0, hcnt);
 
-        scores_mfma<<<dim3(Z * 64), blk, 0, stream>>>(qz[0], qz[1], kz[0], kz[1], S, Z);
+        scores_mfma<<<dim3(Z * 32), blk5, 0, stream>>>(qz[0], qz[1], kz[0], kz[1], S, Z);
         softmax_split<<<dim3(Z * 1024), blk, 0, stream>>>(S);
-        pv_mfma<<<dim3(Z * 64), blk, 0, stream>>>(
+        pv_mfma<<<dim3(Z * 32), blk5, 0, stream>>>(
             (const _Float16*)S, vT[0], vT[1], vT[2], vT[3],
             rcs[0], rcs[1], rcs[2], rcs[3], h0, hcnt, Z);
     }
 
-    final_mfma<<<dim3(32, 4, KS), blk, 0, stream>>>(
+    final_mfma<<<dim3(32, 2, KS), blk5, 0, stream>>>(
         rcs[0], rcs[1], rcs[2], rcs[3], woT[0], woT[1], pbuf);
     final_combine<<<dim3(2048), blk, 0, stream>>>(pbuf, bo, out, KS);
 }
```

Result: slower. 619.6 us (+6.9%).
